# Kernel tuning notes

Measured on AMD Instinct MI355X. Metric: run time of the kernel, lower is better.

Reference implementation:

```python
import jax, jax.numpy as jnp
import numpy as np

B, T, W = 4, 2048, 1024
K, G = 7, 8            # kernel_size, groups
Cg = W // G            # channels per group
SE_R = 16              # SE reduction ratio
LN_EPS = 1e-5


def setup_inputs() -> dict:
    key = jax.random.key(0)
    ks = jax.random.split(key, 8)
    h = jax.random.normal(ks[0], (B, T, W), jnp.float32)
    # mask: True = padding; valid prefix of random length per row
    lengths = jax.random.randint(ks[1], (B,), T // 2, T + 1)
    mask = jnp.arange(T)[None, :] >= lengths[:, None]
    s_w = np.float32(1.0 / np.sqrt(W))
    return dict(
        h=h,
        mask=mask,
        offset_w=jax.random.normal(ks[2], (W, K), jnp.float32) * 0.01,
        offset_b=jnp.zeros((K,), jnp.float32),
        conv_w=jax.random.normal(ks[3], (G, Cg, Cg, K), jnp.float32) * np.float32(1.0 / np.sqrt(Cg * K)),
        conv_b=jnp.zeros((W,), jnp.float32),
        ln_g=jnp.ones((W,), jnp.float32),
        ln_b=jnp.zeros((W,), jnp.float32),
        se_w1=jax.random.normal(ks[4], (W, W // SE_R), jnp.float32) * s_w,
        se_b1=jnp.zeros((W // SE_R,), jnp.float32),
        se_w2=jax.random.normal(ks[5], (W // SE_R, W), jnp.float32) * np.float32(1.0 / np.sqrt(W // SE_R)),
        se_b2=jnp.zeros((W,), jnp.float32),
        proj_w=jax.random.normal(ks[6], (W, 1), jnp.float32) * s_w,
        proj_b=jnp.zeros((1,), jnp.float32),
    )


def deform_conv1d(h, offset_w, offset_b, conv_w, conv_b):
    # h: [B,T,W]. Learned per-(position, tap) fractional offsets; linear interp gather;
    # grouped conv combine. conv_w: [G, out_per_group, in_per_group, K].
    Bn, Tn, Wn = h.shape
    pad = (K - 1) // 2
    offsets = h @ offset_w + offset_b                                   # [B,T,K]
    base = (jnp.arange(Tn, dtype=jnp.float32)[None, :, None]
            + (jnp.arange(K, dtype=jnp.float32) - pad)[None, None, :])  # [1,T,K]
    pos = jnp.clip(base + offsets, 0.0, Tn - 1.0)                       # [B,T,K]
    p0 = jnp.floor(pos).astype(jnp.int32)
    p1 = jnp.minimum(p0 + 1, Tn - 1)
    frac = (pos - p0.astype(jnp.float32))[..., None]                    # [B,T,K,1]
    gather = jax.vmap(lambda hb, ib: hb[ib])                            # [T,W],[T,K] -> [T,K,W]
    sampled = gather(h, p0) * (1.0 - frac) + gather(h, p1) * frac       # [B,T,K,W]
    sg = sampled.reshape(Bn, Tn, K, G, Cg)
    out = jnp.einsum('btkgc,gock->btgo', sg, conv_w).reshape(Bn, Tn, Wn)
    return out + conv_b


def layer_norm(x, g, b):
    mu = jnp.mean(x, axis=-1, keepdims=True)
    var = jnp.mean(jnp.square(x - mu), axis=-1, keepdims=True)
    return (x - mu) * jax.lax.rsqrt(var + LN_EPS) * g + b


def se_block(x, mask, w1, b1, w2, b2):
    valid = (~mask).astype(x.dtype)[..., None]                          # [B,T,1]
    lengths = jnp.clip(jnp.sum(valid, axis=1), 1.0)                     # [B,1]
    s = jnp.sum(x * valid, axis=1) / lengths                            # [B,W]
    gate = jax.nn.sigmoid(jax.nn.relu(s @ w1 + b1) @ w2 + b2)           # [B,W]
    return x * gate[:, None, :]


def reference(h, mask, offset_w, offset_b, conv_w, conv_b, ln_g, ln_b,
              se_w1, se_b1, se_w2, se_b2, proj_w, proj_b):
    x = layer_norm(deform_conv1d(h, offset_w, offset_b, conv_w, conv_b), ln_g, ln_b)
    x = se_block(x, mask, se_w1, se_b1, se_w2, se_b2)
    # dropout: identity in eval mode (p handled outside reference)
    valid = (~mask).astype(x.dtype)[..., None]
    x = x * valid                                                       # masked_fill(mask, 0)
    lengths = jnp.clip(jnp.sum(valid, axis=1), 1.0)                     # [B,1]
    pooled = jnp.sum(x, axis=1) / lengths                               # [B,W]
    return jnp.squeeze(pooled @ proj_w + proj_b, axis=-1)               # [B]
```

## Files before the change

kernel.cpp:

```cpp
#include <hip/hip_runtime.h>
#include <hip/hip_bf16.h>

#define Bdim 4
#define Tdim 2048
#define Wdim 1024
#define Kdim 7
#define Gdim 8
#define Cg   128
#define Hdim 64
#define TT   128

typedef __attribute__((ext_vector_type(8))) short short8v;
typedef __attribute__((ext_vector_type(4))) float float4v;

__device__ __forceinline__ short f2bf(float x) {
    union { float f; unsigned u; } v; v.f = x;
    unsigned r = v.u + 0x7fff + ((v.u >> 16) & 1);
    return (short)(r >> 16);
}

__global__ __launch_bounds__(256) void k_pre(const float* __restrict__ conv_w,
                                             short* __restrict__ Wtb,
                                             const float* __restrict__ h,
                                             const float* __restrict__ offset_w,
                                             const float* __restrict__ offset_b,
                                             int* __restrict__ p0a,
                                             float* __restrict__ fra) {
    int tid = threadIdx.x;
    if (blockIdx.x < 448) {
        int i = blockIdx.x * 256 + tid;
        if (i >= Gdim * Kdim * Cg * 16) return;
        int cb = i & 15;
        int o = (i >> 4) & 127;
        int gk = i >> 11;
        int k = gk % Kdim, g = gk / Kdim;
        const float* src = conv_w + ((size_t)(g * Cg + o) * Cg + cb * 8) * Kdim + k;
        short8v pk;
#pragma unroll
        for (int j = 0; j < 8; j++) pk[j] = f2bf(src[(size_t)j * Kdim]);
        short8v* Wtb8 = (short8v*)Wtb;
        Wtb8[(size_t)gk * 2048 + o * 16 + (cb ^ (o & 7))] = pk;
        return;
    }
    int bt = blockIdx.x - 448;
    int t = bt & (Tdim - 1);
    const float* row = h + (size_t)bt * Wdim;
    float4 hv = *(const float4*)(row + tid * 4);
    const float* ow = offset_w + (size_t)tid * 4 * Kdim;
    float acc[Kdim];
#pragma unroll
    for (int k = 0; k < Kdim; k++)
        acc[k] = hv.x * ow[k] + hv.y * ow[Kdim + k] + hv.z * ow[2 * Kdim + k] + hv.w * ow[3 * Kdim + k];

    __shared__ float wred[4][Kdim];
    int lane = tid & 63, wv = tid >> 6;
#pragma unroll
    for (int k = 0; k < Kdim; k++) {
        float v = acc[k];
#pragma unroll
        for (int off = 32; off > 0; off >>= 1) v += __shfl_down(v, off);
        if (lane == 0) wred[wv][k] = v;
    }
    __syncthreads();
    if (tid < Kdim) {
        float o = wred[0][tid] + wred[1][tid] + wred[2][tid] + wred[3][tid] + offset_b[tid];
        float base = (float)t + (float)(tid - 3);
        float pos = fminf(fmaxf(base + o, 0.f), (float)(Tdim - 1));
        float p0f = floorf(pos);
        p0a[bt * Kdim + tid] = (int)p0f;
        fra[bt * Kdim + tid] = pos - p0f;
    }
}

__global__ __launch_bounds__(512) void k_conv(const float* __restrict__ h,
                                              const short* __restrict__ Wtb,
                                              const float* __restrict__ conv_b,
                                              const int* __restrict__ p0a,
                                              const float* __restrict__ fra,
                                              float* __restrict__ y) {
    __shared__ short8v sA8[TT * 16];
    __shared__ short8v sB8[Cg * 16];

    int blk = blockIdx.x;
    int g = blk & 7;
    int tc = (blk >> 3) & 15;
    int b = blk >> 7;
    int t0 = tc * TT;
    int tid = threadIdx.x;
    int lane = tid & 63, wv = tid >> 6;
    int wt = wv & 3, wo = wv >> 2;
    int r15 = lane & 15, q = lane >> 4;
    int sw = r15 & 7;

    float4v acc[2][4];
#pragma unroll
    for (int tt = 0; tt < 2; tt++)
#pragma unroll
        for (int n = 0; n < 4; n++) acc[tt][n] = (float4v){0.f, 0.f, 0.f, 0.f};

    const float* hg = h + (size_t)b * Tdim * Wdim + g * Cg;
    const short8v* wgB = (const short8v*)Wtb + (size_t)(g * Kdim) * 2048;

    for (int k = 0; k < Kdim; k++) {
        __syncthreads();
#pragma unroll
        for (int i = 0; i < 4; i++) {
            int u = tid + i * 512;
            int r = u >> 4, cb = u & 15;
            int idx = (b * Tdim + t0 + r) * Kdim + k;
            int p0 = p0a[idx];
            float f = fra[idx];
            int p1 = min(p0 + 1, Tdim - 1);
            const float* s0p = hg + (size_t)p0 * Wdim + cb * 8;
            const float* s1p = hg + (size_t)p1 * Wdim + cb * 8;
            float4 a0 = *(const float4*)s0p;
            float4 a1 = *(const float4*)(s0p + 4);
            float4 b0 = *(const float4*)s1p;
            float4 b1 = *(const float4*)(s1p + 4);
            short8v pk;
            pk[0] = f2bf(a0.x + f * (b0.x - a0.x));
            pk[1] = f2bf(a0.y + f * (b0.y - a0.y));
            pk[2] = f2bf(a0.z + f * (b0.z - a0.z));
            pk[3] = f2bf(a0.w + f * (b0.w - a0.w));
            pk[4] = f2bf(a1.x + f * (b1.x - a1.x));
            pk[5] = f2bf(a1.y + f * (b1.y - a1.y));
            pk[6] = f2bf(a1.z + f * (b1.z - a1.z));
            pk[7] = f2bf(a1.w + f * (b1.w - a1.w));
            sA8[r * 16 + (cb ^ (r & 7))] = pk;
        }
        const short8v* wk = wgB + (size_t)k * 2048;
#pragma unroll
        for (int i = 0; i < 4; i++) {
            int u = tid + i * 512;
            sB8[u] = wk[u];
        }
        __syncthreads();
#pragma unroll
        for (int kk = 0; kk < 4; kk++) {
            int cs = kk * 4 + q;
            short8v a0 = sA8[(wt * 32 + r15) * 16 + (cs ^ sw)];
            short8v a1 = sA8[(wt * 32 + 16 + r15) * 16 + (cs ^ sw)];
#pragma unroll
            for (int n = 0; n < 4; n++) {
                int orow = wo * 64 + n * 16 + r15;
                short8v bfv = sB8[orow * 16 + (cs ^ sw)];
                acc[0][n] = __builtin_amdgcn_mfma_f32_16x16x32_bf16(a0, bfv, acc[0][n], 0, 0, 0);
                acc[1][n] = __builtin_amdgcn_mfma_f32_16x16x32_bf16(a1, bfv, acc[1][n], 0, 0, 0);
            }
        }
    }
    int trow0 = t0 + wt * 32 + q * 4;
#pragma unroll
    for (int n = 0; n < 4; n++) {
        int o = wo * 64 + n * 16 + r15;
        float bias = conv_b[g * Cg + o];
#pragma unroll
        for (int tt = 0; tt < 2; tt++) {
            float* yp = y + ((size_t)(b * Tdim + trow0 + tt * 16)) * Wdim + g * Cg + o;
#pragma unroll
            for (int j = 0; j < 4; j++)
                yp[(size_t)j * Wdim] = acc[tt][n][j] + bias;
        }
    }
}

__global__ __launch_bounds__(256) void k_lnpool(const float* __restrict__ y,
                                                const int* __restrict__ mask,
                                                float* __restrict__ partial) {
    int bc = blockIdx.x;
    int b = bc >> 7, ch = bc & 127;
    int t0 = ch * 16;
    int tid = threadIdx.x;
    int lane = tid & 63, wv = tid >> 6;
    __shared__ float rs[4], rq[4];
    __shared__ float smu, sinv;
    float4 acc = {0, 0, 0, 0};
    for (int i = 0; i < 16; i++) {
        int t = t0 + i;
        if (mask[b * Tdim + t]) continue;
        float4 v = *(const float4*)(y + (size_t)(b * Tdim + t) * Wdim + tid * 4);
        float s = v.x + v.y + v.z + v.w;
        float qq = v.x * v.x + v.y * v.y + v.z * v.z + v.w * v.w;
#pragma unroll
        for (int off = 32; off > 0; off >>= 1) { s += __shfl_down(s, off); qq += __shfl_down(qq, off); }
        if (lane == 0) { rs[wv] = s; rq[wv] = qq; }
        __syncthreads();
        if (tid == 0) {
            float S = rs[0] + rs[1] + rs[2] + rs[3];
            float Q = rq[0] + rq[1] + rq[2] + rq[3];
            float mu = S * (1.f / Wdim);
            smu = mu;
            sinv = rsqrtf(Q * (1.f / Wdim) - mu * mu + 1e-5f);
        }
        __syncthreads();
        float mu = smu, inv = sinv;
        acc.x += (v.x - mu) * inv;
        acc.y += (v.y - mu) * inv;
        acc.z += (v.z - mu) * inv;
        acc.w += (v.w - mu) * inv;
    }
    *(float4*)(partial + (size_t)bc * Wdim + tid * 4) = acc;
}

__global__ __launch_bounds__(256) void k_sefinal(const float* __restrict__ partial,
                                                 const int* __restrict__ mask,
                                                 const float* __restrict__ ln_g,
                                                 const float* __restrict__ ln_b,
                                                 const float* __restrict__ w1,
                                                 const float* __restrict__ b1,
                                                 const float* __restrict__ w2,
                                                 const float* __restrict__ b2,
                                                 const float* __restrict__ projw,
                                                 const float* __restrict__ projb,
                                                 float* __restrict__ out) {
    int b = blockIdx.x, tid = threadIdx.x;
    __shared__ float s[Wdim];
    __shared__ float hred[4][Hdim];
    __shared__ float hid[Hdim];
    __shared__ float rbuf[4];
    __shared__ float sLinv;
    int lane = tid & 63, wv = tid >> 6;

    int cnt = 0;
    for (int t = tid; t < Tdim; t += 256) cnt += (mask[b * Tdim + t] ? 0 : 1);
    float fc = (float)cnt;
#pragma unroll
    for (int off = 32; off > 0; off >>= 1) fc += __shfl_down(fc, off);
    if (lane == 0) rbuf[wv] = fc;
    __syncthreads();
    if (tid == 0) {
        float L = rbuf[0] + rbuf[1] + rbuf[2] + rbuf[3];
        sLinv = 1.f / fmaxf(L, 1.f);
    }
    __syncthreads();
    float Linv = sLinv;

    int w4 = tid * 4;
    float4 a = {0, 0, 0, 0};
    for (int chh = 0; chh < 128; chh++) {
        float4 p = *(const float4*)(partial + ((size_t)(b * 128 + chh)) * Wdim + w4);
        a.x += p.x; a.y += p.y; a.z += p.z; a.w += p.w;
    }
    float4 gg = *(const float4*)(ln_g + w4);
    float4 bb = *(const float4*)(ln_b + w4);
    s[w4 + 0] = gg.x * (a.x * Linv) + bb.x;
    s[w4 + 1] = gg.y * (a.y * Linv) + bb.y;
    s[w4 + 2] = gg.z * (a.z * Linv) + bb.z;
    s[w4 + 3] = gg.w * (a.w * Linv) + bb.w;
    __syncthreads();

    int j = tid & 63, p = tid >> 6;
    float ha = 0.f;
    for (int w = p * 256; w < (p + 1) * 256; ++w) ha += s[w] * w1[(size_t)w * Hdim + j];
    hred[p][j] = ha;
    __syncthreads();
    if (tid < Hdim)
        hid[tid] = fmaxf(hred[0][tid] + hred[1][tid] + hred[2][tid] + hred[3][tid] + b1[tid], 0.f);
    __syncthreads();

    float part = 0.f;
    for (int w = tid; w < Wdim; w += 256) {
        float ga = b2[w];
#pragma unroll 8
        for (int j2 = 0; j2 < Hdim; j2++) ga += hid[j2] * w2[(size_t)j2 * Wdim + w];
        float gate = 1.f / (1.f + expf(-ga));
        part += s[w] * gate * projw[w];
    }
#pragma unroll
    for (int off = 32; off > 0; off >>= 1) part += __shfl_down(part, off);
    __syncthreads();
    if (lane == 0) rbuf[wv] = part;
    __syncthreads();
    if (tid == 0) out[b] = rbuf[0] + rbuf[1] + rbuf[2] + rbuf[3] + projb[0];
}

extern "C" void kernel_launch(void* const* d_in, const int* in_sizes, int n_in,
                              void* d_out, int out_size, void* d_ws, size_t ws_size,
                              hipStream_t stream) {
    const float* h        = (const float*)d_in[0];
    const int*   mask     = (const int*)d_in[1];
    const float* offset_w = (const float*)d_in[2];
    const float* offset_b = (const float*)d_in[3];
    const float* conv_w   = (const float*)d_in[4];
    const float* conv_b   = (const float*)d_in[5];
    const float* ln_g     = (const float*)d_in[6];
    const float* ln_b     = (const float*)d_in[7];
    const float* se_w1    = (const float*)d_in[8];
    const float* se_b1    = (const float*)d_in[9];
    const float* se_w2    = (const float*)d_in[10];
    const float* se_b2    = (const float*)d_in[11];
    const float* proj_w   = (const float*)d_in[12];
    const float* proj_b   = (const float*)d_in[13];
    float* out = (float*)d_out;

    char* wsb = (char*)d_ws;
    int*   p0a     = (int*)(wsb);
    float* fra     = (float*)(wsb + 229376);
    short* Wtb     = (short*)(wsb + 458752);
    float* y       = (float*)(wsb + 2293760);
    float* partial = (float*)(wsb + 35848192);

    k_pre<<<dim3(448 + Bdim * Tdim), dim3(256), 0, stream>>>(conv_w, Wtb, h, offset_w, offset_b,
                                                             p0a, fra);
    k_conv<<<dim3(Bdim * (Tdim / TT) * Gdim), dim3(512), 0, stream>>>(h, Wtb, conv_b, p0a, fra, y);
    k_lnpool<<<dim3(Bdim * 128), dim3(256), 0, stream>>>(y, mask, partial);
    k_sefinal<<<dim3(Bdim), dim3(256), 0, stream>>>(partial, mask, ln_g, ln_b,
                                                    se_w1, se_b1, se_w2, se_b2,
                                                    proj_w, proj_b, out);
}
```

Baseline: 115.8 us.

## Store activations in bf16, gather directly into MFMA fragments, atomic pooled reduction

The pre kernel now handles one row per wave without shared-memory reduction, writes a bf16 copy of h, and stores clamped float positions. The conv kernel gathers interpolated bf16 rows straight into MFMA register fragments instead of staging them in shared memory. It double-buffers weight tiles, splits output channels across two blocks, and writes y in bf16. LN-pool uses wave-level stats and atomics into a single per-batch sum, replacing the 128-way partial buffer. This halves gather and y traffic but adds bf16 rounding of h and y, plus nondeterministic atomic summation.

Result: slower. 126.6 us (+9.3%).

```diff
diff --git a/kernel.cpp b/kernel.cpp
--- a/kernel.cpp
+++ b/kernel.cpp
@@ -19,13 +19,33 @@
     return (short)(r >> 16);
 }
 
+__device__ __forceinline__ short8v lerp_pack(uint4 a, uint4 b, float f) {
+    union { uint4 u; short8v s; } r;
+    const unsigned* pa = (const unsigned*)&a;
+    const unsigned* pb = (const unsigned*)&b;
+    unsigned* pr = (unsigned*)&r.u;
+#pragma unroll
+    for (int d = 0; d < 4; d++) {
+        float alo = __uint_as_float(pa[d] << 16);
+        float ahi = __uint_as_float(pa[d] & 0xffff0000u);
+        float blo = __uint_as_float(pb[d] << 16);
+        float bhi = __uint_as_float(pb[d] & 0xffff0000u);
+        float rlo = alo + f * (blo - alo);
+        float rhi = ahi + f * (bhi - ahi);
+        unsigned ulo = __float_as_uint(rlo) + 0x8000u;
+        unsigned uhi = __float_as_uint(rhi) + 0x8000u;
+        pr[d] = __builtin_amdgcn_perm(uhi, ulo, 0x07060302u);
+    }
+    return r.s;
+}
+
 __global__ __launch_bounds__(256) void k_pre(const float* __restrict__ conv_w,
                                              short* __restrict__ Wtb,
                                              const float* __restrict__ h,
                                              const float* __restrict__ offset_w,
                                              const float* __restrict__ offset_b,
-                                             int* __restrict__ p0a,
-                                             float* __restrict__ fra) {
+                                             float* __restrict__ pos,
+                                             ushort* __restrict__ h16) {
     int tid = threadIdx.x;
     if (blockIdx.x < 448) {
         int i = blockIdx.x * 256 + tid;
@@ -42,55 +62,68 @@
         Wtb8[(size_t)gk * 2048 + o * 16 + (cb ^ (o & 7))] = pk;
         return;
     }
-    int bt = blockIdx.x - 448;
+    int lane = tid & 63, wv = tid >> 6;
+    int bt = (blockIdx.x - 448) * 4 + wv;
     int t = bt & (Tdim - 1);
     const float* row = h + (size_t)bt * Wdim;
-    float4 hv = *(const float4*)(row + tid * 4);
-    const float* ow = offset_w + (size_t)tid * 4 * Kdim;
     float acc[Kdim];
 #pragma unroll
-    for (int k = 0; k < Kdim; k++)
-        acc[k] = hv.x * ow[k] + hv.y * ow[Kdim + k] + hv.z * ow[2 * Kdim + k] + hv.w * ow[3 * Kdim + k];
-
-    __shared__ float wred[4][Kdim];
-    int lane = tid & 63, wv = tid >> 6;
+    for (int k = 0; k < Kdim; k++) acc[k] = 0.f;
+#pragma unroll
+    for (int j = 0; j < 4; j++) {
+        int c = lane * 4 + j * 256;
+        float4 hv = *(const float4*)(row + c);
+        const float* ow = offset_w + (size_t)c * Kdim;
+#pragma unroll
+        for (int k = 0; k < Kdim; k++)
+            acc[k] += hv.x * ow[k] + hv.y * ow[Kdim + k] + hv.z * ow[2 * Kdim + k]
+                    + hv.w * ow[3 * Kdim + k];
+        ushort4 hp;
+        hp.x = (ushort)f2bf(hv.x); hp.y = (ushort)f2bf(hv.y);
+        hp.z = (ushort)f2bf(hv.z); hp.w = (ushort)f2bf(hv.w);
+        *(ushort4*)(h16 + (size_t)bt * Wdim + c) = hp;
+    }
 #pragma unroll
     for (int k = 0; k < Kdim; k++) {
-        float v = acc[k];
-#pragma unroll
-        for (int off = 32; off > 0; off >>= 1) v += __shfl_down(v, off);
-        if (lane == 0) wred[wv][k] = v;
-    }
-    __syncthreads();
-    if (tid < Kdim) {
-        float o = wred[0][tid] + wred[1][tid] + wred[2][tid] + wred[3][tid] + offset_b[tid];
-        float base = (float)t + (float)(tid - 3);
-        float pos = fminf(fmaxf(base + o, 0.f), (float)(Tdim - 1));
-        float p0f = floorf(pos);
-        p0a[bt * Kdim + tid] = (int)p0f;
-        fra[bt * Kdim + tid] = pos - p0f;
-    }
-}
-
-__global__ __launch_bounds__(512) void k_conv(const float* __restrict__ h,
-                                              const short* __restrict__ Wtb,
-                                              const float* __restrict__ conv_b,
-                                              const int* __restrict__ p0a,
-                                              const float* __restrict__ fra,
-                                              float* __restrict__ y) {
-    __shared__ short8v sA8[TT * 16];
-    __shared__ short8v sB8[Cg * 16];
+#pragma unroll
+        for (int m = 32; m > 0; m >>= 1) acc[k] += __shfl_xor(acc[k], m);
+    }
+    if (lane < Kdim) {
+        float o = acc[lane] + offset_b[lane];
+        float base = (float)t + (float)(lane - 3);
+        float p = fminf(fmaxf(base + o, 0.f), (float)(Tdim - 1));
+        pos[bt * Kdim + lane] = p;
+    }
+}
+
+__global__ __launch_bounds__(256, 4) void k_conv(const ushort* __restrict__ h16,
+                                                 const short* __restrict__ Wtb,
+                                                 const float* __restrict__ conv_b,
+                                                 const float* __restrict__ pos,
+                                                 ushort* __restrict__ y16) {
+    __shared__ short8v sB8[2][64 * 16];
 
     int blk = blockIdx.x;
-    int g = blk & 7;
-    int tc = (blk >> 3) & 15;
-    int b = blk >> 7;
+    int oh = blk & 1;
+    int g  = (blk >> 1) & 7;
+    int tc = (blk >> 4) & 15;
+    int b  = blk >> 8;
     int t0 = tc * TT;
     int tid = threadIdx.x;
     int lane = tid & 63, wv = tid >> 6;
-    int wt = wv & 3, wo = wv >> 2;
     int r15 = lane & 15, q = lane >> 4;
-    int sw = r15 & 7;
+
+    int rowA = t0 + wv * 32 + r15;
+    int rowB = rowA + 16;
+    float posA[Kdim], posB[Kdim];
+    const float* pA = pos + (b * Tdim + rowA) * Kdim;
+    const float* pB = pos + (b * Tdim + rowB) * Kdim;
+#pragma unroll
+    for (int k = 0; k < Kdim; k++) { posA[k] = pA[k]; posB[k] = pB[k]; }
+
+    const ushort* hb = h16 + (size_t)(b * Tdim) * Wdim + g * Cg;
+    const short8v* WtbV = (const short8v*)Wtb;
+#define WK(kk_) (WtbV + (((size_t)(g * Kdim + (kk_)) * 128 + oh * 64) << 4))
 
     float4v acc[2][4];
 #pragma unroll
@@ -98,111 +131,145 @@
 #pragma unroll
         for (int n = 0; n < 4; n++) acc[tt][n] = (float4v){0.f, 0.f, 0.f, 0.f};
 
-    const float* hg = h + (size_t)b * Tdim * Wdim + g * Cg;
-    const short8v* wgB = (const short8v*)Wtb + (size_t)(g * Kdim) * 2048;
-
+    {
+        const short8v* wk = WK(0);
+        short8v st[4];
+#pragma unroll
+        for (int i = 0; i < 4; i++) st[i] = wk[i * 256 + tid];
+#pragma unroll
+        for (int i = 0; i < 4; i++) sB8[0][i * 256 + tid] = st[i];
+    }
+
+#pragma unroll 1
     for (int k = 0; k < Kdim; k++) {
         __syncthreads();
-#pragma unroll
-        for (int i = 0; i < 4; i++) {
-            int u = tid + i * 512;
-            int r = u >> 4, cb = u & 15;
-            int idx = (b * Tdim + t0 + r) * Kdim + k;
-            int p0 = p0a[idx];
-            float f = fra[idx];
-            int p1 = min(p0 + 1, Tdim - 1);
-            const float* s0p = hg + (size_t)p0 * Wdim + cb * 8;
-            const float* s1p = hg + (size_t)p1 * Wdim + cb * 8;
-            float4 a0 = *(const float4*)s0p;
-            float4 a1 = *(const float4*)(s0p + 4);
-            float4 b0 = *(const float4*)s1p;
-            float4 b1 = *(const float4*)(s1p + 4);
-            short8v pk;
-            pk[0] = f2bf(a0.x + f * (b0.x - a0.x));
-            pk[1] = f2bf(a0.y + f * (b0.y - a0.y));
-            pk[2] = f2bf(a0.z + f * (b0.z - a0.z));
-            pk[3] = f2bf(a0.w + f * (b0.w - a0.w));
-            pk[4] = f2bf(a1.x + f * (b1.x - a1.x));
-            pk[5] = f2bf(a1.y + f * (b1.y - a1.y));
-            pk[6] = f2bf(a1.z + f * (b1.z - a1.z));
-            pk[7] = f2bf(a1.w + f * (b1.w - a1.w));
-            sA8[r * 16 + (cb ^ (r & 7))] = pk;
-        }
-        const short8v* wk = wgB + (size_t)k * 2048;
-#pragma unroll
-        for (int i = 0; i < 4; i++) {
-            int u = tid + i * 512;
-            sB8[u] = wk[u];
-        }
-        __syncthreads();
+        int cur = k & 1;
+        float pv0 = posA[k];
+        int p00 = (int)pv0; float f0 = pv0 - (float)p00;
+        int p01 = min(p00 + 1, Tdim - 1);
+        const uint4* r00 = (const uint4*)(hb + (size_t)p00 * Wdim);
+        const uint4* r01 = (const uint4*)(hb + (size_t)p01 * Wdim);
+        uint4 a0[4], a1[4];
+#pragma unroll
+        for (int kk = 0; kk < 4; kk++) {
+            int u = kk * 4 + q;
+            a0[kk] = r00[u];
+            a1[kk] = r01[u];
+        }
+        short8v st[4];
+        if (k < Kdim - 1) {
+            const short8v* wk = WK(k + 1);
+#pragma unroll
+            for (int i = 0; i < 4; i++) st[i] = wk[i * 256 + tid];
+        }
+        short8v frg0[4];
+#pragma unroll
+        for (int kk = 0; kk < 4; kk++) frg0[kk] = lerp_pack(a0[kk], a1[kk], f0);
+        float pv1 = posB[k];
+        int p10 = (int)pv1; float f1 = pv1 - (float)p10;
+        int p11 = min(p10 + 1, Tdim - 1);
+        const uint4* r10 = (const uint4*)(hb + (size_t)p10 * Wdim);
+        const uint4* r11 = (const uint4*)(hb + (size_t)p11 * Wdim);
+#pragma unroll
+        for (int kk = 0; kk < 4; kk++) {
+            int u = kk * 4 + q;
+            a0[kk] = r10[u];
+            a1[kk] = r11[u];
+        }
+        short8v frg1[4];
+#pragma unroll
+        for (int kk = 0; kk < 4; kk++) frg1[kk] = lerp_pack(a0[kk], a1[kk], f1);
 #pragma unroll
         for (int kk = 0; kk < 4; kk++) {
             int cs = kk * 4 + q;
-            short8v a0 = sA8[(wt * 32 + r15) * 16 + (cs ^ sw)];
-            short8v a1 = sA8[(wt * 32 + 16 + r15) * 16 + (cs ^ sw)];
 #pragma unroll
             for (int n = 0; n < 4; n++) {
-                int orow = wo * 64 + n * 16 + r15;
-                short8v bfv = sB8[orow * 16 + (cs ^ sw)];
-                acc[0][n] = __builtin_amdgcn_mfma_f32_16x16x32_bf16(a0, bfv, acc[0][n], 0, 0, 0);
-                acc[1][n] = __builtin_amdgcn_mfma_f32_16x16x32_bf16(a1, bfv, acc[1][n], 0, 0, 0);
+                int orow = n * 16 + r15;
+                short8v bf = sB8[cur][orow * 16 + (cs ^ (orow & 7))];
+                acc[0][n] = __builtin_amdgcn_mfma_f32_16x16x32_bf16(frg0[kk], bf, acc[0][n], 0, 0, 0);
+                acc[1][n] = __builtin_amdgcn_mfma_f32_16x16x32_bf16(frg1[kk], bf, acc[1][n], 0, 0, 0);
             }
         }
-    }
-    int trow0 = t0 + wt * 32 + q * 4;
+        if (k < Kdim - 1) {
+#pragma unroll
+            for (int i = 0; i < 4; i++) sB8[cur ^ 1][i * 256 + tid] = st[i];
+        }
+    }
 #pragma unroll
     for (int n = 0; n < 4; n++) {
-        int o = wo * 64 + n * 16 + r15;
-        float bias = conv_b[g * Cg + o];
+        int col = g * Cg + oh * 64 + n * 16 + r15;
+        float bias = conv_b[col];
 #pragma unroll
         for (int tt = 0; tt < 2; tt++) {
-            float* yp = y + ((size_t)(b * Tdim + trow0 + tt * 16)) * Wdim + g * Cg + o;
+            int trow = t0 + wv * 32 + tt * 16 + q * 4;
 #pragma unroll
             for (int j = 0; j < 4; j++)
-                yp[(size_t)j * Wdim] = acc[tt][n][j] + bias;
-        }
-    }
-}
-
-__global__ __launch_bounds__(256) void k_lnpool(const float* __restrict__ y,
+                y16[(size_t)(b * Tdim + trow + j) * Wdim + col] =
+                    (ushort)f2bf(acc[tt][n][j] + bias);
+        }
+    }
+}
+
+__global__ __launch_bounds__(256) void k_lnpool(const ushort* __restrict__ y16,
                                                 const int* __restrict__ mask,
-                                                float* __restrict__ partial) {
-    int bc = blockIdx.x;
-    int b = bc >> 7, ch = bc & 127;
-    int t0 = ch * 16;
+                                                float* __restrict__ s_sum) {
+    int blk = blockIdx.x;
+    int b = blk >> 6, ch = blk & 63;
     int tid = threadIdx.x;
     int lane = tid & 63, wv = tid >> 6;
-    __shared__ float rs[4], rq[4];
-    __shared__ float smu, sinv;
-    float4 acc = {0, 0, 0, 0};
-    for (int i = 0; i < 16; i++) {
-        int t = t0 + i;
+    __shared__ float red[4 * Wdim];
+
+    float accv[2][8];
+#pragma unroll
+    for (int j = 0; j < 2; j++)
+#pragma unroll
+        for (int e = 0; e < 8; e++) accv[j][e] = 0.f;
+
+    for (int i = 0; i < 8; i++) {
+        int t = ch * 32 + wv * 8 + i;
         if (mask[b * Tdim + t]) continue;
-        float4 v = *(const float4*)(y + (size_t)(b * Tdim + t) * Wdim + tid * 4);
-        float s = v.x + v.y + v.z + v.w;
-        float qq = v.x * v.x + v.y * v.y + v.z * v.z + v.w * v.w;
-#pragma unroll
-        for (int off = 32; off > 0; off >>= 1) { s += __shfl_down(s, off); qq += __shfl_down(qq, off); }
-        if (lane == 0) { rs[wv] = s; rq[wv] = qq; }
-        __syncthreads();
-        if (tid == 0) {
-            float S = rs[0] + rs[1] + rs[2] + rs[3];
-            float Q = rq[0] + rq[1] + rq[2] + rq[3];
-            float mu = S * (1.f / Wdim);
-            smu = mu;
-            sinv = rsqrtf(Q * (1.f / Wdim) - mu * mu + 1e-5f);
-        }
-        __syncthreads();
-        float mu = smu, inv = sinv;
-        acc.x += (v.x - mu) * inv;
-        acc.y += (v.y - mu) * inv;
-        acc.z += (v.z - mu) * inv;
-        acc.w += (v.w - mu) * inv;
-    }
-    *(float4*)(partial + (size_t)bc * Wdim + tid * 4) = acc;
-}
-
-__global__ __launch_bounds__(256) void k_sefinal(const float* __restrict__ partial,
+        const ushort* yr = y16 + (size_t)(b * Tdim + t) * Wdim;
+        float v[2][8];
+        float s = 0.f, qq = 0.f;
+#pragma unroll
+        for (int j = 0; j < 2; j++) {
+            uint4 u = *(const uint4*)(yr + lane * 8 + j * 512);
+            const unsigned* pu = (const unsigned*)&u;
+#pragma unroll
+            for (int d = 0; d < 4; d++) {
+                float lo = __uint_as_float(pu[d] << 16);
+                float hi = __uint_as_float(pu[d] & 0xffff0000u);
+                v[j][d * 2] = lo; v[j][d * 2 + 1] = hi;
+                s += lo + hi; qq += lo * lo + hi * hi;
+            }
+        }
+#pragma unroll
+        for (int m = 32; m > 0; m >>= 1) { s += __shfl_xor(s, m); qq += __shfl_xor(qq, m); }
+        float mu = s * (1.f / Wdim);
+        float inv = rsqrtf(qq * (1.f / Wdim) - mu * mu + 1e-5f);
+#pragma unroll
+        for (int j = 0; j < 2; j++)
+#pragma unroll
+            for (int e = 0; e < 8; e++) accv[j][e] += (v[j][e] - mu) * inv;
+    }
+#pragma unroll
+    for (int j = 0; j < 2; j++)
+        *(float4*)(&red[wv * Wdim + lane * 8 + j * 512]) =
+            (float4){accv[j][0], accv[j][1], accv[j][2], accv[j][3]};
+#pragma unroll
+    for (int j = 0; j < 2; j++)
+        *(float4*)(&red[wv * Wdim + lane * 8 + j * 512 + 4]) =
+            (float4){accv[j][4], accv[j][5], accv[j][6], accv[j][7]};
+    __syncthreads();
+#pragma unroll
+    for (int e = 0; e < 4; e++) {
+        int w = tid + e * 256;
+        float a = red[w] + red[Wdim + w] + red[2 * Wdim + w] + red[3 * Wdim + w];
+        atomicAdd(&s_sum[b * Wdim + w], a);
+    }
+}
+
+__global__ __launch_bounds__(256) void k_sefinal(const float* __restrict__ s_sum,
                                                  const int* __restrict__ mask,
                                                  const float* __restrict__ ln_g,
                                                  const float* __restrict__ ln_b,
@@ -236,11 +303,7 @@
     float Linv = sLinv;
 
     int w4 = tid * 4;
-    float4 a = {0, 0, 0, 0};
-    for (int chh = 0; chh < 128; chh++) {
-        float4 p = *(const float4*)(partial + ((size_t)(b * 128 + chh)) * Wdim + w4);
-        a.x += p.x; a.y += p.y; a.z += p.z; a.w += p.w;
-    }
+    float4 a = *(const float4*)(s_sum + b * Wdim + w4);
     float4 gg = *(const float4*)(ln_g + w4);
     float4 bb = *(const float4*)(ln_b + w4);
     s[w4 + 0] = gg.x * (a.x * Linv) + bb.x;
@@ -294,17 +357,19 @@
     float* out = (float*)d_out;
 
     char* wsb = (char*)d_ws;
-    int*   p0a     = (int*)(wsb);
-    float* fra     = (float*)(wsb + 229376);
-    short* Wtb     = (short*)(wsb + 458752);
-    float* y       = (float*)(wsb + 2293760);
-    float* partial = (float*)(wsb + 35848192);
-
-    k_pre<<<dim3(448 + Bdim * Tdim), dim3(256), 0, stream>>>(conv_w, Wtb, h, offset_w, offset_b,
-                                                             p0a, fra);
-    k_conv<<<dim3(Bdim * (Tdim / TT) * Gdim), dim3(512), 0, stream>>>(h, Wtb, conv_b, p0a, fra, y);
-    k_lnpool<<<dim3(Bdim * 128), dim3(256), 0, stream>>>(y, mask, partial);
-    k_sefinal<<<dim3(Bdim), dim3(256), 0, stream>>>(partial, mask, ln_g, ln_b,
+    float*  pos   = (float*)(wsb);
+    ushort* h16   = (ushort*)(wsb + 229376);
+    short*  Wtb   = (short*)(wsb + 17006592);
+    ushort* y16   = (ushort*)(wsb + 18841600);
+    float*  s_sum = (float*)(wsb + 35618816);
+
+    hipMemsetAsync(s_sum, 0, Bdim * Wdim * sizeof(float), stream);
+    k_pre<<<dim3(448 + Bdim * Tdim / 4), dim3(256), 0, stream>>>(conv_w, Wtb, h, offset_w,
+                                                                 offset_b, pos, h16);
+    k_conv<<<dim3(Bdim * (Tdim / TT) * Gdim * 2), dim3(256), 0, stream>>>(h16, Wtb, conv_b,
+                                                                          pos, y16);
+    k_lnpool<<<dim3(Bdim * 64), dim3(256), 0, stream>>>(y16, mask, s_sum);
+    k_sefinal<<<dim3(Bdim), dim3(256), 0, stream>>>(s_sum, mask, ln_g, ln_b,
                                                     se_w1, se_b1, se_w2, se_b2,
                                                     proj_w, proj_b, out);
 }
```
